# Kernel optimization log

Hardware: AMD Instinct MI355X
Metric: run time of the kernel (lower is better)

The kernel has to match this reference:

```python
import jax, jax.numpy as jnp
import numpy as np

B, N, D, H = 2048, 512, 128, 256
TRADE_K, N_BEST, CONF_TH = 10, 50, 0.05


def setup_inputs() -> dict:
    key = jax.random.key(0)
    ks = jax.random.split(key, 5)
    return {
        "signal_features": jax.random.normal(ks[0], (B, N, D), jnp.float32),
        "spread": jax.random.uniform(ks[1], (B, N), jnp.float32, minval=1e-4, maxval=0.01),
        "volatility": jax.random.uniform(ks[2], (B, N), jnp.float32, minval=1e-4, maxval=0.05),
        "W1": jax.random.normal(ks[3], (D, H), jnp.float32) / np.sqrt(D).astype(np.float32),
        "b1": jnp.zeros((H,), jnp.float32),
        "W2": jax.random.normal(ks[4], (H, 1), jnp.float32) / np.sqrt(H).astype(np.float32),
        "b2": jnp.zeros((1,), jnp.float32),
    }


def _scatter_mask(idx, n):
    # idx: [B, k] int32 -> bool mask [B, n] with True at idx positions
    b = idx.shape[0]
    return jnp.zeros((b, n), bool).at[jnp.arange(b)[:, None], idx].set(True)


def reference(signal_features, spread, volatility, W1, b1, W2, b2):
    # signal predictor: per-asset MLP with sigmoid head -> [B, N]
    h = jax.nn.relu(jnp.einsum('bnd,dh->bnh', signal_features, W1) + b1)
    signal_repr = jax.nn.sigmoid(jnp.einsum('bnh,ho->bno', h, W2)[..., 0] + b2[0])
    ls_score = signal_repr - 0.5  # allow_short_positions=True

    n_best = min(N_BEST, N)
    valid_spread = jnp.isfinite(spread) & (spread > 0)
    ratio = jnp.where(valid_spread, volatility / (spread + 1e-8), -jnp.inf)
    _, best_idx = jax.lax.top_k(ratio, n_best)
    universe_mask = _scatter_mask(best_idx, N)
    # rows with no valid spread: whole universe allowed
    universe_mask = universe_mask | ~valid_spread.any(axis=1, keepdims=True)

    masked_abs = jnp.where(universe_mask, jnp.abs(ls_score), -jnp.inf)
    k = min(TRADE_K, n_best)
    _, top_idx = jax.lax.top_k(masked_abs, k)
    mask = _scatter_mask(top_idx, N)

    selected = jnp.where(mask, ls_score, 0.0)
    action = selected / (jnp.sum(jnp.abs(selected), axis=1, keepdims=True) + 1e-8)

    confidence = masked_abs.max(axis=1)
    confidence = jnp.where(jnp.isfinite(confidence), confidence, 0.0)
    take_trade = (confidence >= CONF_TH).astype(action.dtype)[:, None]
    action = action * take_trade
    return action, confidence
```

## Files before the change

kernel.cpp:

```cpp
#include <hip/hip_runtime.h>
#include <hip/hip_bf16.h>
#include <math.h>

#define B_ 2048
#define N_ 512
#define D_ 128
#define H_ 256
#define BANDf 2e-4f

typedef __attribute__((ext_vector_type(8))) short bf16x8;
typedef __attribute__((ext_vector_type(4))) float f32x4;

__device__ __forceinline__ short f2bf(float x) {
    unsigned u = __float_as_uint(x);
    u = u + 0x7fffu + ((u >> 16) & 1u);
    return (short)(u >> 16);
}
__device__ __forceinline__ float bf2f(short h) {
    return __uint_as_float(((unsigned)(unsigned short)h) << 16);
}
__device__ __forceinline__ unsigned cvt_pk_bf16(float a, float b) {
    unsigned r;
    asm("v_cvt_pk_bf16_f32 %0, %1, %2" : "=v"(r) : "v"(a), "v"(b));
    return r;
}
template<int K>
__device__ __forceinline__ float dpp_shr_add(float zz) {
    int s = __builtin_amdgcn_update_dpp(0, __float_as_int(zz), 0x110 | K, 0xf, 0xf, true);
    return zz + __int_as_float(s);
}

__global__ __launch_bounds__(256) void pack_w(const float* __restrict__ W1,
                                              short* __restrict__ WpH,
                                              short* __restrict__ WpL)
{
    int tid = blockIdx.x * 256 + threadIdx.x;
    int l  = tid & 63;
    int ks = (tid >> 6) & 3;
    int nf = tid >> 8;
    int n  = nf * 16 + (l & 15);
    int kb = ks * 32 + ((l >> 4) << 3);
    bf16x8 hi, lo;
    #pragma unroll
    for (int j = 0; j < 8; ++j) {
        float w = W1[(size_t)(kb + j) * H_ + n];
        short h = f2bf(w);
        hi[j] = h;
        lo[j] = f2bf(w - bf2f(h));
    }
    *(bf16x8*)&WpH[(size_t)tid * 8] = hi;
    *(bf16x8*)&WpL[(size_t)tid * 8] = lo;
}

__global__ __launch_bounds__(256, 3) void mlp_mfma(
    const float* __restrict__ X, const short* __restrict__ WpH,
    const short* __restrict__ WpL, const float* __restrict__ b1,
    const float* __restrict__ W2, const float* __restrict__ b2,
    float* __restrict__ ls)
{
    __shared__ short Xh[64 * 128];
    __shared__ short Xl[64 * 128];
    __shared__ float zl[256];

    const int t    = threadIdx.x;
    const int lane = t & 63;
    const int wn   = t >> 6;
    const size_t m0 = (size_t)blockIdx.x * 64;

    const bf16x8* WH = (const bf16x8*)WpH;
    const bf16x8* WL = (const bf16x8*)WpL;

    bf16x8 Bh[2][4], Bl[2][4];
    #pragma unroll
    for (int q = 0; q < 4; ++q) {
        Bh[0][q] = WH[((wn * 4 + q) * 4 + 0) * 64 + lane];
        Bl[0][q] = WL[((wn * 4 + q) * 4 + 0) * 64 + lane];
    }

    {
        const float4* Xg = (const float4*)(X + m0 * D_);
        #pragma unroll
        for (int i = 0; i < 8; ++i) {
            int f = t + i * 256;
            float4 v = Xg[f];
            int row = f >> 5, k0 = (f & 31) << 2;
            unsigned h01 = cvt_pk_bf16(v.x, v.y);
            unsigned h23 = cvt_pk_bf16(v.z, v.w);
            float l0 = v.x - __uint_as_float(h01 << 16);
            float l1 = v.y - __uint_as_float(h01 & 0xffff0000u);
            float l2 = v.z - __uint_as_float(h23 << 16);
            float l3 = v.w - __uint_as_float(h23 & 0xffff0000u);
            unsigned lo01 = cvt_pk_bf16(l0, l1);
            unsigned lo23 = cvt_pk_bf16(l2, l3);
            int sidx = (row * 128 + k0) ^ ((row & 7) << 3);
            *(uint2*)&Xh[sidx] = make_uint2(h01, h23);
            *(uint2*)&Xl[sidx] = make_uint2(lo01, lo23);
        }
    }
    __syncthreads();

    f32x4 acc[4][4];
    #pragma unroll
    for (int mf = 0; mf < 4; ++mf)
        #pragma unroll
        for (int q = 0; q < 4; ++q)
            acc[mf][q] = (f32x4){0.f, 0.f, 0.f, 0.f};

    __builtin_amdgcn_s_setprio(1);
    #pragma unroll
    for (int ks = 0; ks < 4; ++ks) {
        const int cur = ks & 1, nxt = cur ^ 1;
        if (ks < 3) {
            #pragma unroll
            for (int q = 0; q < 4; ++q) {
                Bh[nxt][q] = WH[((wn * 4 + q) * 4 + ks + 1) * 64 + lane];
                Bl[nxt][q] = WL[((wn * 4 + q) * 4 + ks + 1) * 64 + lane];
            }
        }
        #pragma unroll
        for (int mf = 0; mf < 4; ++mf) {
            int r = mf * 16 + (lane & 15);
            int sidx = (r * 128 + ks * 32 + ((lane >> 4) << 3)) ^ ((r & 7) << 3);
            bf16x8 Ah = *(const bf16x8*)&Xh[sidx];
            bf16x8 Al = *(const bf16x8*)&Xl[sidx];
            #pragma unroll
            for (int q = 0; q < 4; ++q) {
                acc[mf][q] = __builtin_amdgcn_mfma_f32_16x16x32_bf16(Ah, Bh[cur][q], acc[mf][q], 0, 0, 0);
                acc[mf][q] = __builtin_amdgcn_mfma_f32_16x16x32_bf16(Al, Bh[cur][q], acc[mf][q], 0, 0, 0);
                acc[mf][q] = __builtin_amdgcn_mfma_f32_16x16x32_bf16(Ah, Bl[cur][q], acc[mf][q], 0, 0, 0);
            }
        }
    }
    __builtin_amdgcn_s_setprio(0);

    float b1v[4], w2v[4];
    #pragma unroll
    for (int q = 0; q < 4; ++q) {
        int c = wn * 64 + q * 16 + (lane & 15);
        b1v[q] = b1[c];
        w2v[q] = W2[c];
    }
    #pragma unroll
    for (int mf = 0; mf < 4; ++mf) {
        #pragma unroll
        for (int i = 0; i < 4; ++i) {
            float zz = 0.f;
            #pragma unroll
            for (int q = 0; q < 4; ++q) {
                float h = acc[mf][q][i] + b1v[q];
                h = h > 0.f ? h : 0.f;
                zz += h * w2v[q];
            }
            zz = dpp_shr_add<1>(zz);
            zz = dpp_shr_add<2>(zz);
            zz = dpp_shr_add<4>(zz);
            zz = dpp_shr_add<8>(zz);
            if ((lane & 15) == 15) zl[wn * 64 + mf * 16 + ((lane >> 4) << 2) + i] = zz;
        }
    }
    __syncthreads();
    if (t < 64) {
        float z = zl[t] + zl[64 + t] + zl[128 + t] + zl[192 + t] + b2[0];
        ls[m0 + t] = 1.f / (1.f + expf(-z)) - 0.5f;
    }
}

__device__ __forceinline__ unsigned f2key(float f) {
    unsigned u = __float_as_uint(f);
    return (u & 0x80000000u) ? ~u : (u | 0x80000000u);
}
__device__ __forceinline__ float key2f(unsigned k) {
    return __uint_as_float((k & 0x80000000u) ? (k & 0x7fffffffu) : ~k);
}
__device__ __forceinline__ int lane_lt_count(unsigned long long m) {
    return __builtin_amdgcn_mbcnt_hi((unsigned)(m >> 32),
           __builtin_amdgcn_mbcnt_lo((unsigned)m, 0));
}

__device__ __forceinline__ void radix_topk(const unsigned (&key)[8], int k,
                                           unsigned &T, int &need)
{
    unsigned prefix = 0, maskhi = 0;
    int kk = k;
    for (int bit = 31; bit >= 0; --bit) {
        unsigned b = 1u << bit;
        int cnt1 = 0;
        #pragma unroll
        for (int j = 0; j < 8; ++j) {
            bool one = ((key[j] & maskhi) == prefix) && (key[j] & b);
            cnt1 += __popcll(__ballot(one));
        }
        if (cnt1 >= kk) prefix |= b; else kk -= cnt1;
        maskhi |= b;
    }
    T = prefix; need = kk;
}

__device__ __forceinline__ void tie_member(const unsigned (&key)[8], unsigned T,
                                           int need, bool (&mem)[8])
{
    int base = 0;
    #pragma unroll
    for (int j = 0; j < 8; ++j) {
        unsigned long long eb = __ballot(key[j] == T);
        int r = base + lane_lt_count(eb);
        mem[j] = (key[j] > T) || ((key[j] == T) && (r < need));
        base += __popcll(eb);
    }
}

__global__ __launch_bounds__(256) void select_kernel(
    const float* __restrict__ ls, const float* __restrict__ spread,
    const float* __restrict__ vol, const float* __restrict__ X,
    const float* __restrict__ W1, const float* __restrict__ b1,
    const float* __restrict__ W2, const float* __restrict__ b2,
    float* __restrict__ action, float* __restrict__ conf_out)
{
    const int t = threadIdx.x;
    const int l = t & 63;
    const int w = t >> 6;
    const int b = blockIdx.x * 4 + w;
    const size_t base = (size_t)b * N_;

    float rv[8], lsv[8];
    unsigned kr[8];
    bool anyv = false;
    #pragma unroll
    for (int j = 0; j < 8; ++j) {
        int n = l + (j << 6);
        float sp = spread[base + n];
        float vo = vol[base + n];
        bool valid = isfinite(sp) && (sp > 0.f);
        rv[j]  = valid ? (vo / (sp + 1e-8f)) : -INFINITY;
        lsv[j] = ls[base + n];
        anyv |= valid;
        kr[j] = f2key(rv[j]);
    }
    bool allow_all = (__any((int)anyv) == 0);

    unsigned T50; int need50;
    radix_topk(kr, 50, T50, need50);
    bool mem50[8];
    tie_member(kr, T50, need50, mem50);

    float mabs[8];
    unsigned km[8];
    #pragma unroll
    for (int j = 0; j < 8; ++j) {
        bool u = allow_all || mem50[j];
        mabs[j] = u ? fabsf(lsv[j]) : -INFINITY;
        km[j] = f2key(mabs[j]);
    }
    unsigned T10; int need10;
    radix_topk(km, 10, T10, need10);
    bool mem10[8];
    tie_member(km, T10, need10, mem10);
    float b10 = key2f(T10);

    float zp = 0.f, cf = -INFINITY;
    #pragma unroll
    for (int j = 0; j < 8; ++j) {
        if (mem10[j]) zp += mabs[j];
        cf = fmaxf(cf, mabs[j]);
    }
    #pragma unroll
    for (int s = 1; s < 64; s <<= 1) {
        zp += __shfl_xor(zp, s, 64);
        cf = fmaxf(cf, __shfl_xor(cf, s, 64));
    }
    float conf = cf;

    bool confclose = fabsf(conf - 0.05f) <= BANDf;
    bool inband[8];
    int nb = 0;
    #pragma unroll
    for (int j = 0; j < 8; ++j) {
        inband[j] = (mabs[j] != -INFINITY) && (fabsf(mabs[j] - b10) <= BANDf);
        nb += __popcll(__ballot(inband[j]));
    }
    bool redo = (nb >= 2) || confclose;

    if (!redo) {
        float cfin  = isfinite(conf) ? conf : 0.f;
        float scale = (cfin >= 0.05f) ? (1.f / (zp + 1e-8f)) : 0.f;
        #pragma unroll
        for (int j = 0; j < 8; ++j) {
            int n = l + (j << 6);
            action[base + n] = mem10[j] ? lsv[j] * scale : 0.f;
        }
        if (l == 0) conf_out[b] = cfin;
        return;
    }

    const float2* xr2 = (const float2*)&X[base * D_];
    float4 bb = *(const float4*)&b1[l * 4];
    float4 ww = *(const float4*)&W2[l * 4];
    const float b2v = b2[0];

    #pragma unroll
    for (int j = 0; j < 8; ++j) {
        bool cand = (nb >= 2 && inband[j]) || (confclose && mabs[j] == conf);
        unsigned long long bal = __ballot(cand);
        while (bal) {
            int s = __ffsll((long long)bal) - 1;
            bal &= bal - 1;
            int asset = s + (j << 6);
            float2 x2 = xr2[(size_t)asset * 64 + l];
            float h0 = 0.f, h1 = 0.f, h2 = 0.f, h3 = 0.f;
            #pragma unroll 16
            for (int kk = 0; kk < D_; ++kk) {
                float xk = __shfl((kk & 1) ? x2.y : x2.x, kk >> 1, 64);
                float4 wv = *(const float4*)&W1[(size_t)kk * H_ + l * 4];
                h0 += xk * wv.x; h1 += xk * wv.y; h2 += xk * wv.z; h3 += xk * wv.w;
            }
            h0 += bb.x; h1 += bb.y; h2 += bb.z; h3 += bb.w;
            float zz = (h0 > 0.f ? h0 : 0.f) * ww.x + (h1 > 0.f ? h1 : 0.f) * ww.y
                     + (h2 > 0.f ? h2 : 0.f) * ww.z + (h3 > 0.f ? h3 : 0.f) * ww.w;
            #pragma unroll
            for (int sh = 1; sh < 64; sh <<= 1) zz += __shfl_xor(zz, sh, 64);
            float val = 1.f / (1.f + expf(-(zz + b2v))) - 0.5f;
            if (l == s) {
                lsv[j]  = val;
                mabs[j] = fabsf(val);
                km[j]   = f2key(mabs[j]);
            }
        }
    }

    unsigned T10b; int need10b;
    radix_topk(km, 10, T10b, need10b);
    bool mem10b[8];
    tie_member(km, T10b, need10b, mem10b);

    float zx = 0.f, cfx = -INFINITY;
    #pragma unroll
    for (int j = 0; j < 8; ++j) {
        if (mem10b[j]) zx += mabs[j];
        cfx = fmaxf(cfx, mabs[j]);
    }
    #pragma unroll
    for (int s = 1; s < 64; s <<= 1) {
        zx += __shfl_xor(zx, s, 64);
        cfx = fmaxf(cfx, __shfl_xor(cfx, s, 64));
    }
    cfx = isfinite(cfx) ? cfx : 0.f;
    float scale = (cfx >= 0.05f) ? (1.f / (zx + 1e-8f)) : 0.f;
    #pragma unroll
    for (int j = 0; j < 8; ++j) {
        int n = l + (j << 6);
        action[base + n] = mem10b[j] ? lsv[j] * scale : 0.f;
    }
    if (l == 0) conf_out[b] = cfx;
}

extern "C" void kernel_launch(void* const* d_in, const int* in_sizes, int n_in,
                              void* d_out, int out_size, void* d_ws, size_t ws_size,
                              hipStream_t stream)
{
    const float* X  = (const float*)d_in[0];
    const float* sp = (const float*)d_in[1];
    const float* vo = (const float*)d_in[2];
    const float* W1 = (const float*)d_in[3];
    const float* b1 = (const float*)d_in[4];
    const float* W2 = (const float*)d_in[5];
    const float* b2 = (const float*)d_in[6];

    float* action = (float*)d_out;
    float* conf   = action + (size_t)B_ * N_;

    float* ls = (float*)d_ws;
    size_t need = (size_t)B_ * N_ * 4 + 2 * (size_t)D_ * H_ * 2;
    short *WpH, *WpL;
    if (ws_size >= need) {
        WpH = (short*)((char*)d_ws + (size_t)B_ * N_ * 4);
        WpL = WpH + (size_t)D_ * H_;
    } else {
        WpH = (short*)(action + (size_t)out_size - 2 * (size_t)D_ * H_ / 2);
        WpL = WpH + (size_t)D_ * H_;
    }

    hipLaunchKernelGGL(pack_w, dim3(16), dim3(256), 0, stream, W1, WpH, WpL);
    hipLaunchKernelGGL(mlp_mfma, dim3((B_ * N_) / 64), dim3(256), 0, stream,
                       X, WpH, WpL, b1, W2, b2, ls);
    hipLaunchKernelGGL(select_kernel, dim3(B_ / 4), dim3(256), 0, stream,
                       ls, sp, vo, X, W1, b1, W2, b2, action, conf);
}
```

Measured before the change: 279.6 us.

## Move universe top-50 selection into extra MLP grid blocks

Appends 512 blocks to the MLP launch that compute the per-row spread/volatility top-50 universe mask. The result is stored as 64-bit ballot bitmasks plus an all-invalid flag in workspace. The select kernel then reads the bitmasks instead of redoing the radix top-k, so this latency-bound serial work runs alongside the compute-heavy MLP rather than after it. The cost is extra workspace traffic and a fallback path for when the workspace is too small. It also risks imbalance if the extra blocks are scheduled last.

```diff
diff --git a/kernel.cpp b/kernel.cpp
--- a/kernel.cpp
+++ b/kernel.cpp
@@ -7,6 +7,8 @@
 #define D_ 128
 #define H_ 256
 #define BANDf 2e-4f
+#define NMLP (B_ * N_ / 64)
+#define NUNI (B_ / 4)
 
 typedef __attribute__((ext_vector_type(8))) short bf16x8;
 typedef __attribute__((ext_vector_type(4))) float f32x4;
@@ -28,6 +30,50 @@
 __device__ __forceinline__ float dpp_shr_add(float zz) {
     int s = __builtin_amdgcn_update_dpp(0, __float_as_int(zz), 0x110 | K, 0xf, 0xf, true);
     return zz + __int_as_float(s);
+}
+
+__device__ __forceinline__ unsigned f2key(float f) {
+    unsigned u = __float_as_uint(f);
+    return (u & 0x80000000u) ? ~u : (u | 0x80000000u);
+}
+__device__ __forceinline__ float key2f(unsigned k) {
+    return __uint_as_float((k & 0x80000000u) ? (k & 0x7fffffffu) : ~k);
+}
+__device__ __forceinline__ int lane_lt_count(unsigned long long m) {
+    return __builtin_amdgcn_mbcnt_hi((unsigned)(m >> 32),
+           __builtin_amdgcn_mbcnt_lo((unsigned)m, 0));
+}
+
+__device__ __forceinline__ void radix_topk(const unsigned (&key)[8], int k,
+                                           unsigned &T, int &need)
+{
+    unsigned prefix = 0, maskhi = 0;
+    int kk = k;
+    for (int bit = 31; bit >= 0; --bit) {
+        unsigned b = 1u << bit;
+        int cnt1 = 0;
+        #pragma unroll
+        for (int j = 0; j < 8; ++j) {
+            bool one = ((key[j] & maskhi) == prefix) && (key[j] & b);
+            cnt1 += __popcll(__ballot(one));
+        }
+        if (cnt1 >= kk) prefix |= b; else kk -= cnt1;
+        maskhi |= b;
+    }
+    T = prefix; need = kk;
+}
+
+__device__ __forceinline__ void tie_member(const unsigned (&key)[8], unsigned T,
+                                           int need, bool (&mem)[8])
+{
+    int base = 0;
+    #pragma unroll
+    for (int j = 0; j < 8; ++j) {
+        unsigned long long eb = __ballot(key[j] == T);
+        int r = base + lane_lt_count(eb);
+        mem[j] = (key[j] > T) || ((key[j] == T) && (r < need));
+        base += __popcll(eb);
+    }
 }
 
 __global__ __launch_bounds__(256) void pack_w(const float* __restrict__ W1,
@@ -56,15 +102,48 @@
     const float* __restrict__ X, const short* __restrict__ WpH,
     const short* __restrict__ WpL, const float* __restrict__ b1,
     const float* __restrict__ W2, const float* __restrict__ b2,
-    float* __restrict__ ls)
-{
+    float* __restrict__ ls, const float* __restrict__ spread,
+    const float* __restrict__ vol, unsigned long long* __restrict__ uball,
+    int* __restrict__ uflag)
+{
+    const int t    = threadIdx.x;
+    const int lane = t & 63;
+    const int wn   = t >> 6;
+
+    if ((int)blockIdx.x >= NMLP) {
+        const int row = ((int)blockIdx.x - NMLP) * 4 + wn;
+        const size_t base = (size_t)row * N_;
+        float rv[8];
+        unsigned kr[8];
+        bool anyv = false;
+        #pragma unroll
+        for (int j = 0; j < 8; ++j) {
+            int n = lane + (j << 6);
+            float sp = spread[base + n];
+            float vo = vol[base + n];
+            bool valid = isfinite(sp) && (sp > 0.f);
+            rv[j] = valid ? (vo / (sp + 1e-8f)) : -INFINITY;
+            anyv |= valid;
+            kr[j] = f2key(rv[j]);
+        }
+        bool allow_all = (__any((int)anyv) == 0);
+        unsigned T50; int need50;
+        radix_topk(kr, 50, T50, need50);
+        bool mem50[8];
+        tie_member(kr, T50, need50, mem50);
+        #pragma unroll
+        for (int j = 0; j < 8; ++j) {
+            unsigned long long eb = __ballot(mem50[j]);
+            if (lane == 0) uball[((size_t)row << 3) + j] = eb;
+        }
+        if (lane == 0) uflag[row] = allow_all ? 1 : 0;
+        return;
+    }
+
     __shared__ short Xh[64 * 128];
     __shared__ short Xl[64 * 128];
     __shared__ float zl[256];
 
-    const int t    = threadIdx.x;
-    const int lane = t & 63;
-    const int wn   = t >> 6;
     const size_t m0 = (size_t)blockIdx.x * 64;
 
     const bf16x8* WH = (const bf16x8*)WpH;
@@ -165,56 +244,14 @@
     }
 }
 
-__device__ __forceinline__ unsigned f2key(float f) {
-    unsigned u = __float_as_uint(f);
-    return (u & 0x80000000u) ? ~u : (u | 0x80000000u);
-}
-__device__ __forceinline__ float key2f(unsigned k) {
-    return __uint_as_float((k & 0x80000000u) ? (k & 0x7fffffffu) : ~k);
-}
-__device__ __forceinline__ int lane_lt_count(unsigned long long m) {
-    return __builtin_amdgcn_mbcnt_hi((unsigned)(m >> 32),
-           __builtin_amdgcn_mbcnt_lo((unsigned)m, 0));
-}
-
-__device__ __forceinline__ void radix_topk(const unsigned (&key)[8], int k,
-                                           unsigned &T, int &need)
-{
-    unsigned prefix = 0, maskhi = 0;
-    int kk = k;
-    for (int bit = 31; bit >= 0; --bit) {
-        unsigned b = 1u << bit;
-        int cnt1 = 0;
-        #pragma unroll
-        for (int j = 0; j < 8; ++j) {
-            bool one = ((key[j] & maskhi) == prefix) && (key[j] & b);
-            cnt1 += __popcll(__ballot(one));
-        }
-        if (cnt1 >= kk) prefix |= b; else kk -= cnt1;
-        maskhi |= b;
-    }
-    T = prefix; need = kk;
-}
-
-__device__ __forceinline__ void tie_member(const unsigned (&key)[8], unsigned T,
-                                           int need, bool (&mem)[8])
-{
-    int base = 0;
-    #pragma unroll
-    for (int j = 0; j < 8; ++j) {
-        unsigned long long eb = __ballot(key[j] == T);
-        int r = base + lane_lt_count(eb);
-        mem[j] = (key[j] > T) || ((key[j] == T) && (r < need));
-        base += __popcll(eb);
-    }
-}
-
 __global__ __launch_bounds__(256) void select_kernel(
     const float* __restrict__ ls, const float* __restrict__ spread,
     const float* __restrict__ vol, const float* __restrict__ X,
     const float* __restrict__ W1, const float* __restrict__ b1,
     const float* __restrict__ W2, const float* __restrict__ b2,
-    float* __restrict__ action, float* __restrict__ conf_out)
+    float* __restrict__ action, float* __restrict__ conf_out,
+    const unsigned long long* __restrict__ uball,
+    const int* __restrict__ uflag)
 {
     const int t = threadIdx.x;
     const int l = t & 63;
@@ -222,26 +259,37 @@
     const int b = blockIdx.x * 4 + w;
     const size_t base = (size_t)b * N_;
 
-    float rv[8], lsv[8];
-    unsigned kr[8];
-    bool anyv = false;
-    #pragma unroll
-    for (int j = 0; j < 8; ++j) {
-        int n = l + (j << 6);
-        float sp = spread[base + n];
-        float vo = vol[base + n];
-        bool valid = isfinite(sp) && (sp > 0.f);
-        rv[j]  = valid ? (vo / (sp + 1e-8f)) : -INFINITY;
-        lsv[j] = ls[base + n];
-        anyv |= valid;
-        kr[j] = f2key(rv[j]);
-    }
-    bool allow_all = (__any((int)anyv) == 0);
-
-    unsigned T50; int need50;
-    radix_topk(kr, 50, T50, need50);
+    float lsv[8];
+    #pragma unroll
+    for (int j = 0; j < 8; ++j)
+        lsv[j] = ls[base + l + (j << 6)];
+
     bool mem50[8];
-    tie_member(kr, T50, need50, mem50);
+    bool allow_all;
+    if (uball != nullptr) {
+        allow_all = uflag[b] != 0;
+        #pragma unroll
+        for (int j = 0; j < 8; ++j)
+            mem50[j] = (uball[((size_t)b << 3) + j] >> l) & 1ull;
+    } else {
+        float rv[8];
+        unsigned kr[8];
+        bool anyv = false;
+        #pragma unroll
+        for (int j = 0; j < 8; ++j) {
+            int n = l + (j << 6);
+            float sp = spread[base + n];
+            float vo = vol[base + n];
+            bool valid = isfinite(sp) && (sp > 0.f);
+            rv[j] = valid ? (vo / (sp + 1e-8f)) : -INFINITY;
+            anyv |= valid;
+            kr[j] = f2key(rv[j]);
+        }
+        allow_all = (__any((int)anyv) == 0);
+        unsigned T50; int need50;
+        radix_topk(kr, 50, T50, need50);
+        tie_member(kr, T50, need50, mem50);
+    }
 
     float mabs[8];
     unsigned km[8];
@@ -369,19 +417,29 @@
     float* conf   = action + (size_t)B_ * N_;
 
     float* ls = (float*)d_ws;
-    size_t need = (size_t)B_ * N_ * 4 + 2 * (size_t)D_ * H_ * 2;
+    size_t wbytes = 2 * (size_t)D_ * H_ * 2;
+    size_t base_need = (size_t)B_ * N_ * 4 + wbytes;
+    size_t ball_bytes = (size_t)B_ * 8 * 8 + (size_t)B_ * 4;
     short *WpH, *WpL;
-    if (ws_size >= need) {
+    unsigned long long* uball = nullptr;
+    int* uflag = nullptr;
+    if (ws_size >= base_need + ball_bytes) {
+        WpH = (short*)((char*)d_ws + (size_t)B_ * N_ * 4);
+        WpL = WpH + (size_t)D_ * H_;
+        uball = (unsigned long long*)((char*)d_ws + base_need);
+        uflag = (int*)(uball + (size_t)B_ * 8);
+    } else if (ws_size >= base_need) {
         WpH = (short*)((char*)d_ws + (size_t)B_ * N_ * 4);
         WpL = WpH + (size_t)D_ * H_;
     } else {
-        WpH = (short*)(action + (size_t)out_size - 2 * (size_t)D_ * H_ / 2);
+        WpH = (short*)(action + (size_t)out_size - wbytes / 4);
         WpL = WpH + (size_t)D_ * H_;
     }
 
+    const int grid_mlp = (uball != nullptr) ? (NMLP + NUNI) : NMLP;
     hipLaunchKernelGGL(pack_w, dim3(16), dim3(256), 0, stream, W1, WpH, WpL);
-    hipLaunchKernelGGL(mlp_mfma, dim3((B_ * N_) / 64), dim3(256), 0, stream,
-                       X, WpH, WpL, b1, W2, b2, ls);
+    hipLaunchKernelGGL(mlp_mfma, dim3(grid_mlp), dim3(256), 0, stream,
+                       X, WpH, WpL, b1, W2, b2, ls, sp, vo, uball, uflag);
     hipLaunchKernelGGL(select_kernel, dim3(B_ / 4), dim3(256), 0, stream,
-                       ls, sp, vo, X, W1, b1, W2, b2, action, conf);
-}
+                       ls, sp, vo, X, W1, b1, W2, b2, action, conf, uball, uflag);
+}
```

Result: no change. 283.1 us (+1.2%).
